# Kernel optimization log

Hardware: AMD Instinct MI355X
Metric: run time of the kernel (lower is better)

The kernel has to match this reference:

```python
import jax, jax.numpy as jnp
import numpy as np

D_K = 64
NEG = -1000000000.0

def setup_inputs() -> dict:
    key = jax.random.key(0)
    kq, kk, kv, km = jax.random.split(key, 4)
    B, H, S = 2, 16, 2048
    query = jax.random.normal(kq, (B, H, S, D_K), dtype=jnp.float32)
    k_ = jax.random.normal(kk, (B, H, S, D_K), dtype=jnp.float32)
    value = jax.random.normal(kv, (B, H, S, D_K), dtype=jnp.float32)
    mask = jax.random.randint(km, (1, 1, S, S), 0, 2, dtype=jnp.int32)
    return {"query": query, "key": k_, "value": value, "mask": mask}

def reference(query, key, value, mask):
    # scores: [B,H,S,S]
    scale = jnp.asarray(D_K ** 0.5, dtype=query.dtype)
    scores = jnp.einsum('bhqd,bhkd->bhqk', query, key) / scale
    scores = jnp.where(mask == 0, jnp.asarray(NEG, dtype=scores.dtype), scores)
    proba = jax.nn.softmax(scores, axis=-1)
    return jnp.einsum('bhqk,bhkd->bhqd', proba, value)
```

## Files before the change

kernel.cpp:

```cpp
#include <hip/hip_runtime.h>
#include <hip/hip_bf16.h>
#include <stdint.h>


#define SLEN 2048
#define DK 64
#define KVB 64
#define NTG 16
#define MFIX 13.0f
#define VPB 136
#define KIMG 9216
#define VIMG 9216
#define KOFF (512*1024)
#define VOFF (KOFF + 32*32*KIMG)
#define WSNEED ((size_t)VOFF + (size_t)32*32*VIMG)
#define TILEB (KIMG + VIMG)

typedef __attribute__((ext_vector_type(8)))  _Float16 half8;
typedef __attribute__((ext_vector_type(8)))  short    short8;
typedef __attribute__((ext_vector_type(4)))  short    s4v;
typedef __attribute__((ext_vector_type(2)))  unsigned uint2v;
typedef __attribute__((ext_vector_type(16))) float    f32x16;
typedef __attribute__((ext_vector_type(4)))  float    float4v;
typedef __attribute__((ext_vector_type(2)))  float    float2v;
typedef __attribute__((ext_vector_type(4)))  unsigned uint4v;
typedef __attribute__((ext_vector_type(4)))  int      int4v;

static __device__ __forceinline__ float fexp2(float x){
#if __has_builtin(__builtin_amdgcn_exp2f)
  return __builtin_amdgcn_exp2f(x);
#else
  float r; asm("v_exp_f32 %0, %1" : "=v"(r) : "v"(x)); return r;
#endif
}
static __device__ __forceinline__ unsigned pkh(float lo, float hi){
  return __builtin_bit_cast(unsigned, __builtin_amdgcn_cvt_pkrtz(lo, hi));
}
static __device__ __forceinline__ half8 pack8h(float4v a, float4v b, float s){
  uint4v u;
  u[0] = pkh(a[0]*s, a[1]*s);
  u[1] = pkh(a[2]*s, a[3]*s);
  u[2] = pkh(b[0]*s, b[1]*s);
  u[3] = pkh(b[2]*s, b[3]*s);
  return __builtin_bit_cast(half8, u);
}
static __device__ __forceinline__ half8 joinh(s4v a, s4v b){
  return __builtin_bit_cast(half8, __builtin_shufflevector(a, b, 0,1,2,3,4,5,6,7));
}
static __device__ __forceinline__ void gload16(const void* g, void* l){
  __builtin_amdgcn_global_load_lds(
    (const __attribute__((address_space(1))) void*)g,
    (__attribute__((address_space(3))) void*)l, 16, 0, 0);
}

__global__ __launch_bounds__(256)
void ScaledDotAttention_prep(const float* __restrict__ K, const float* __restrict__ V,
                             const int* __restrict__ mask, uint8_t* __restrict__ ws){
  __shared__ float vl[64][65];
  const int bid = blockIdx.x;
  const int i   = threadIdx.x;
  if (bid >= 1024){
    uint32_t* mtw = (uint32_t*)ws;
    int lane = i & 63;
    int wid  = i >> 6;
    int q    = (bid - 1024) * 4 + wid;
    const int* row = mask + (size_t)q * SLEN;
    #pragma unroll 4
    for (int t = 0; t < 32; ++t){
      unsigned long long b = __ballot(row[t*64 + lane] != 0);
      if (lane == 0)
        *(unsigned long long*)(mtw + (size_t)t*4096 + (size_t)q*2) = b;
    }
    return;
  }
  const int bt = bid;
  const float* Kt = K + ((size_t)(bt >> 5)*SLEN + (bt & 31)*KVB)*DK;
  const float* Vt = V + ((size_t)(bt >> 5)*SLEN + (bt & 31)*KVB)*DK;
  uint8_t* Kimg = ws + KOFF + (size_t)bt*KIMG;
  uint8_t* Vimg = ws + VOFF + (size_t)bt*VIMG;
  {
    int d8 = i & 7;
    #pragma unroll
    for (int h = 0; h < 2; ++h){
      int k = (i >> 3) + h*32;
      const float* src = Kt + k*DK + d8*8;
      float4v a = *(const float4v*)src, b = *(const float4v*)(src + 4);
      uint2v w0, w1;
      w0[0] = pkh(a[0], a[1]); w0[1] = pkh(a[2], a[3]);
      w1[0] = pkh(b[0], b[1]); w1[1] = pkh(b[2], b[3]);
      *(uint2v*)(Kimg + k*VPB + d8*16)     = w0;
      *(uint2v*)(Kimg + k*VPB + d8*16 + 8) = w1;
    }
  }
  {
    int k = i >> 2, c4 = (i & 3) * 16;
    const float* src = Vt + k*DK + c4;
    #pragma unroll
    for (int c = 0; c < 4; ++c){
      float4v x = *(const float4v*)(src + c*4);
      vl[k][c4 + c*4 + 0] = x[0]; vl[k][c4 + c*4 + 1] = x[1];
      vl[k][c4 + c*4 + 2] = x[2]; vl[k][c4 + c*4 + 3] = x[3];
    }
  }
  __syncthreads();
  {
    int d = i >> 2, k0 = (i & 3) * 16;
    #pragma unroll
    for (int c = 0; c < 4; ++c){
      uint2v w;
      w[0] = pkh(vl[k0 + c*4 + 0][d], vl[k0 + c*4 + 1][d]);
      w[1] = pkh(vl[k0 + c*4 + 2][d], vl[k0 + c*4 + 3][d]);
      *(uint2v*)(Vimg + d*VPB + k0*2 + c*8) = w;
    }
  }
}

__global__ __launch_bounds__(512, 2)
void ScaledDotAttention_attn_main(const float* __restrict__ Q,
                                  const uint8_t* __restrict__ ws,
                                  float* __restrict__ Out){
  __shared__ alignas(16) char arena[2*2*TILEB];

  const int tid  = threadIdx.x;
  const int lane = tid & 63;
  const int l31  = lane & 31;
  const int hi   = lane >> 5;
  const int wid  = __builtin_amdgcn_readfirstlane(tid >> 6);
  const int g    = wid >> 2;
  const int wq   = wid & 3;

  const int bid = blockIdx.x;
  const int xcd = bid & 7, ii = bid >> 3;
  const int bh  = xcd + 8*(ii & 3);
  const int qt  = ii >> 2;

  const float* Qb = Q + (size_t)bh*SLEN*DK;
  const int qbase = qt*128 + wq*32;
  const float C1 = 0.18033688011112042592f;

  half8 qf[4];
  {
    const float* qrow = Qb + (size_t)(qbase + l31)*DK + hi*8;
    #pragma unroll
    for (int c = 0; c < 4; ++c){
      float4v f0 = *(const float4v*)(qrow + c*16);
      float4v f1 = *(const float4v*)(qrow + c*16 + 4);
      qf[c] = pack8h(f0, f1, C1);
    }
  }

  f32x16 O0, O1;
  #pragma unroll
  for (int r = 0; r < 16; ++r){ O0[r] = 0.f; O1[r] = 0.f; }
  float lsum = 0.f;
  const float vneg = -1.0e9f;

  const uint32_t* mtw = (const uint32_t*)ws;
  auto MLOAD = [&](int it)->uint64_t{
    int kt = g*NTG + it;
    return *(const uint64_t*)(mtw + (size_t)kt*4096 + (size_t)(qbase + l31)*2);
  };

  auto STAGE = [&](int buf, int it){
    int kt = g*NTG + it;
    const uint8_t* Kg = ws + KOFF + (size_t)(bh*32 + kt)*KIMG;
    const uint8_t* Vg = ws + VOFF + (size_t)(bh*32 + kt)*VIMG;
    char* Lk = arena + g*(2*TILEB) + buf*TILEB;
    char* Lv = Lk + KIMG;
    for (int s = wq; s < 9; s += 4) gload16(Kg + s*1024 + lane*16, Lk + s*1024);
    for (int s = wq; s < 9; s += 4) gload16(Vg + s*1024 + lane*16, Lv + s*1024);
  };

  STAGE(0, 0);
  uint64_t wv = MLOAD(0);
  __syncthreads();
  int cur = 0;

  #pragma unroll 1
  for (int it = 0; it < NTG; ++it){
    if (it + 1 < NTG) STAGE(cur ^ 1, it + 1);
    uint64_t wv_next = (it + 1 < NTG) ? MLOAD(it + 1) : 0;

    const char* Klc = arena + g*(2*TILEB) + cur*TILEB;
    const char* Vtc = Klc + KIMG;

    #pragma unroll
    for (int ks = 0; ks < 2; ++ks){
      f32x16 acc;
      #pragma unroll
      for (int r = 0; r < 16; ++r) acc[r] = -MFIX;
      #pragma unroll
      for (int dc = 0; dc < 4; ++dc){
        int rowb = (ks*32 + l31)*VPB + dc*32 + hi*16;
        s4v ka = *(const s4v*)(Klc + rowb);
        s4v kb = *(const s4v*)(Klc + rowb + 8);
        acc = __builtin_amdgcn_mfma_f32_32x32x16_f16(joinh(ka, kb), qf[dc], acc, 0, 0, 0);
      }
      uint32_t w = (uint32_t)(wv >> (32*ks)) >> (4*hi);
      #pragma unroll
      for (int kc = 0; kc < 2; ++kc){
        float p[8];
        #pragma unroll
        for (int j = 0; j < 8; ++j){
          int r = kc*8 + j;
          unsigned bit = (w >> ((r & 3) + 8*(r >> 2))) & 1u;
          p[j] = fexp2(bit ? acc[r] : vneg);
        }
        lsum += ((p[0]+p[1]) + (p[2]+p[3])) + ((p[4]+p[5]) + (p[6]+p[7]));
        uint4v pw;
        pw[0] = pkh(p[0], p[1]);
        pw[1] = pkh(p[2], p[3]);
        pw[2] = pkh(p[4], p[5]);
        pw[3] = pkh(p[6], p[7]);
        half8 pf = __builtin_bit_cast(half8, pw);
        int kbyte = (ks*32 + kc*16 + 4*hi) * 2;
        #pragma unroll
        for (int hf = 0; hf < 2; ++hf){
          int d = hf*32 + l31;
          int base = d*VPB + kbyte;
          s4v a = *(const s4v*)(Vtc + base);
          s4v b = *(const s4v*)(Vtc + base + 16);
          if (hf == 0) O0 = __builtin_amdgcn_mfma_f32_32x32x16_f16(joinh(a, b), pf, O0, 0, 0, 0);
          else         O1 = __builtin_amdgcn_mfma_f32_32x32x16_f16(joinh(a, b), pf, O1, 0, 0, 0);
        }
      }
    }
    wv = wv_next;
    __syncthreads();
    cur ^= 1;
  }

  lsum = lsum + __shfl_xor(lsum, 32, 64);
  float* Mg  = (float*)arena;
  float* smL = (float*)(arena + 128*65*4);

  if (g == 1){
    float* mg = &Mg[(wq*32 + l31)*65];
    #pragma unroll
    for (int r = 0; r < 16; ++r){
      int c0 = (r & 3) + 8*(r >> 2) + 4*hi;
      mg[c0]      = O0[r];
      mg[c0 + 32] = O1[r];
    }
    if (hi == 0) smL[wq*32 + l31] = lsum;
  }
  __syncthreads();
  if (g == 0){
    float lt = lsum + smL[wq*32 + l31];
    float rinv = 1.0f / lt;
    const float* mg = &Mg[(wq*32 + l31)*65];
    float* orow = Out + ((size_t)bh*SLEN + qbase + l31)*DK;
    #pragma unroll
    for (int r = 0; r < 16; ++r){
      int c0 = (r & 3) + 8*(r >> 2) + 4*hi;
      orow[c0]      = (O0[r] + mg[c0])      * rinv;
      orow[c0 + 32] = (O1[r] + mg[c0 + 32]) * rinv;
    }
  }
}

template<bool USE_WS>
__global__ __launch_bounds__(512, 2)
void ScaledDotAttention_attn_fb(const float* __restrict__ Q, const float* __restrict__ K,
                                const float* __restrict__ V, const uint32_t* __restrict__ mtw,
                                const int* __restrict__ mask, float* __restrict__ Out)
{
  __shared__ alignas(16) unsigned short Kl[2][KVB*64];
  __shared__ alignas(16) unsigned short Vt[2][DK*(VPB/2)];
  const int tid  = threadIdx.x;
  const int lane = tid & 63;
  const int l31  = lane & 31;
  const int hi   = lane >> 5;
  const int wid  = __builtin_amdgcn_readfirstlane(tid >> 6);
  const int bid = blockIdx.x;
  const int xcd = bid & 7, ii = bid >> 3;
  const int bh  = xcd + 8*(ii & 3);
  const int qt  = ii >> 2;
  const float* Qb = Q + (size_t)bh*SLEN*DK;
  const float* Kb = K + (size_t)bh*SLEN*DK;
  const float* Vb = V + (size_t)bh*SLEN*DK;
  const int qbase = qt*256 + wid*32;
  const float C1 = 0.18033688011112042592f;
  half8 qf[4];
  {
    const float* qrow = Qb + (size_t)(qbase + l31)*DK + hi*8;
    #pragma unroll
    for (int c = 0; c < 4; ++c){
      float4v f0 = *(const float4v*)(qrow + c*16);
      float4v f1 = *(const float4v*)(qrow + c*16 + 4);
      qf[c] = pack8h(f0, f1, C1);
    }
  }
  f32x16 O0, O1;
  #pragma unroll
  for (int r = 0; r < 16; ++r){ O0[r] = 0.f; O1[r] = 0.f; }
  float lsum = 0.f;
  const float vneg = -1.0e9f;
  const int skr  = tid >> 3;
  const int sc8b = tid & 7;
  const int vd   = (tid & 31) * 2;
  const int vk   = (tid >> 5) * 4;
  float4v ka0, ka1;
  float2v vv0, vv1, vv2, vv3;
  auto LOADT = [&](int it){
    const float* kp = Kb + (size_t)it*KVB*DK + skr*DK + sc8b*8;
    ka0 = *(const float4v*)kp;  ka1 = *(const float4v*)(kp + 4);
    const float* vp = Vb + (size_t)it*KVB*DK + vk*DK + vd;
    vv0 = *(const float2v*)vp;
    vv1 = *(const float2v*)(vp + DK);
    vv2 = *(const float2v*)(vp + 2*DK);
    vv3 = *(const float2v*)(vp + 3*DK);
  };
  auto WRITE = [&](int buf){
    half8 kw = pack8h(ka0, ka1, 1.0f);
    int kaddr = (skr*128 + sc8b*16) ^ ((skr & 7) << 4);
    *(half8*)((char*)&Kl[buf][0] + kaddr) = kw;
    uint2v r0, r1;
    r0[0] = pkh(vv0[0], vv1[0]); r0[1] = pkh(vv2[0], vv3[0]);
    r1[0] = pkh(vv0[1], vv1[1]); r1[1] = pkh(vv2[1], vv3[1]);
    *(uint2v*)((char*)&Vt[buf][0] + vd*VPB + vk*2)     = r0;
    *(uint2v*)((char*)&Vt[buf][0] + (vd+1)*VPB + vk*2) = r1;
  };
  LOADT(0); WRITE(0); LOADT(1);
  __syncthreads();
  int cur = 0;
  #pragma unroll 1
  for (int it = 0; it < 32; ++it){
    if (it + 1 < 32) WRITE(cur ^ 1);
    if (it + 2 < 32) LOADT(it + 2);
    uint64_t wv = 0;
    if constexpr (USE_WS)
      wv = *(const uint64_t*)(mtw + (size_t)it*4096 + (size_t)(qbase + l31)*2);
    const unsigned short* Klc = &Kl[cur][0];
    const unsigned short* Vtc = &Vt[cur][0];
    #pragma unroll
    for (int ks = 0; ks < 2; ++ks){
      f32x16 acc;
      #pragma unroll
      for (int r = 0; r < 16; ++r) acc[r] = -MFIX;
      #pragma unroll
      for (int dc = 0; dc < 4; ++dc){
        int kaddr = ((ks*32 + l31)*128 + dc*32 + hi*16) ^ ((l31 & 7) << 4);
        half8 kf = *(const half8*)((const char*)Klc + kaddr);
        acc = __builtin_amdgcn_mfma_f32_32x32x16_f16(kf, qf[dc], acc, 0, 0, 0);
      }
      float p[16];
      if constexpr (USE_WS){
        uint32_t w = (uint32_t)(wv >> (32*ks)) >> (4*hi);
        #pragma unroll
        for (int r = 0; r < 16; ++r){
          unsigned bit = (w >> ((r & 3) + 8*(r >> 2))) & 1u;
          p[r] = fexp2(bit ? acc[r] : vneg);
        }
      } else {
        const int* mri = mask + (size_t)(qbase + l31)*SLEN + it*KVB + ks*32 + 4*hi;
        int4v g0 = *(const int4v*)(mri);
        int4v g1 = *(const int4v*)(mri + 8);
        int4v g2 = *(const int4v*)(mri + 16);
        int4v g3 = *(const int4v*)(mri + 24);
        #pragma unroll
        for (int r = 0; r < 16; ++r){
          int gi = r >> 2;
          int gv = (gi==0 ? g0[r&3] : gi==1 ? g1[r&3] : gi==2 ? g2[r&3] : g3[r&3]);
          p[r] = fexp2(gv ? acc[r] : vneg);
        }
      }
      float q0 = (p[0]+p[1]) + (p[2]+p[3]);
      float q1 = (p[4]+p[5]) + (p[6]+p[7]);
      float q2 = (p[8]+p[9]) + (p[10]+p[11]);
      float q3 = (p[12]+p[13]) + (p[14]+p[15]);
      lsum += (q0+q1) + (q2+q3);
      #pragma unroll
      for (int kc = 0; kc < 2; ++kc){
        uint4v pw;
        pw[0] = pkh(p[8*kc+0], p[8*kc+1]);
        pw[1] = pkh(p[8*kc+2], p[8*kc+3]);
        pw[2] = pkh(p[8*kc+4], p[8*kc+5]);
        pw[3] = pkh(p[8*kc+6], p[8*kc+7]);
        half8 pf = __builtin_bit_cast(half8, pw);
        int kbyte = (ks*32 + kc*16 + 4*hi) * 2;
        #pragma unroll
        for (int hf = 0; hf < 2; ++hf){
          int d = hf*32 + l31;
          int base = d*VPB + kbyte;
          s4v a = *(const s4v*)((const char*)Vtc + base);
          s4v b = *(const s4v*)((const char*)Vtc + base + 16);
          if (hf == 0) O0 = __builtin_amdgcn_mfma_f32_32x32x16_f16(joinh(a, b), pf, O0, 0, 0, 0);
          else         O1 = __builtin_amdgcn_mfma_f32_32x32x16_f16(joinh(a, b), pf, O1, 0, 0, 0);
        }
      }
    }
    __syncthreads();
    cur ^= 1;
  }
  float lt = lsum + __shfl_xor(lsum, 32, 64);
  float rinv = 1.0f / lt;
  float* orow = Out + ((size_t)bh*SLEN + qbase + l31)*DK;
  #pragma unroll
  for (int r = 0; r < 16; ++r){
    int c0 = (r & 3) + 8*(r >> 2) + 4*hi;
    orow[c0]      = O0[r] * rinv;
    orow[c0 + 32] = O1[r] * rinv;
  }
}

extern "C" void kernel_launch(void* const* d_in, const int* in_sizes, int n_in,
                              void* d_out, int out_size, void* d_ws, size_t ws_size,
                              hipStream_t stream) {
  const float* Q    = (const float*)d_in[0];
  const float* K    = (const float*)d_in[1];
  const float* V    = (const float*)d_in[2];
  const int*   mask = (const int*)d_in[3];
  float* Out = (float*)d_out;

  if (ws_size >= WSNEED) {
    uint8_t* ws = (uint8_t*)d_ws;
    ScaledDotAttention_prep<<<dim3(1536), dim3(256), 0, stream>>>(K, V, mask, ws);
    ScaledDotAttention_attn_main<<<dim3(512), dim3(512), 0, stream>>>(Q, ws, Out);
  } else if (ws_size >= (size_t)(SLEN/64) * SLEN * 2 * sizeof(uint32_t)) {
    uint32_t* mtw = (uint32_t*)d_ws;
    ScaledDotAttention_prep<<<dim3(1536), dim3(256), 0, stream>>>(K, V, mask, (uint8_t*)mtw);
    ScaledDotAttention_attn_fb<true><<<dim3(256), dim3(512), 0, stream>>>(Q, K, V, mtw, mask, Out);
  } else {
    ScaledDotAttention_attn_fb<false><<<dim3(256), dim3(512), 0, stream>>>(Q, K, V, (const uint32_t*)nullptr, mask, Out);
  }
}
```

Measured before the change: 73.57 us.

## Expand mask to fp16 bit-masks and apply via AND on packed probabilities

Adds a path, used when the workspace is large enough, that expands the int mask into per-element 16-bit all-ones/zero words. The attention kernel then exponentiates unconditionally and ANDs the packed fp16 probabilities with these words, and sums them with a dot2 instruction. This replaces the per-element bit extraction and select, and shortens the row-sum reduction. In exchange the mask becomes an 8 MB array that every head re-reads through the cache. The change also raises wave priority around the MFMA blocks with s_setprio, and restructures the PV loads to index both V halves from one base address.

```diff
diff --git a/kernel.cpp b/kernel.cpp
--- a/kernel.cpp
+++ b/kernel.cpp
@@ -11,12 +11,15 @@
 #define VPB 136
 #define KIMG 9216
 #define VIMG 9216
-#define KOFF (512*1024)
-#define VOFF (KOFF + 32*32*KIMG)
-#define WSNEED ((size_t)VOFF + (size_t)32*32*VIMG)
+#define MEXPB ((size_t)SLEN*1024*4)
+#define IMGB  ((size_t)32*32*(KIMG+VIMG))
+#define WSBIG (MEXPB + IMGB)
+#define WSMID ((size_t)512*1024 + IMGB)
+#define WSBITS ((size_t)(SLEN/64)*SLEN*2*sizeof(uint32_t))
 #define TILEB (KIMG + VIMG)
 
 typedef __attribute__((ext_vector_type(8)))  _Float16 half8;
+typedef __attribute__((ext_vector_type(2)))  _Float16 half2v;
 typedef __attribute__((ext_vector_type(8)))  short    short8;
 typedef __attribute__((ext_vector_type(4)))  short    s4v;
 typedef __attribute__((ext_vector_type(2)))  unsigned uint2v;
@@ -47,37 +50,58 @@
 static __device__ __forceinline__ half8 joinh(s4v a, s4v b){
   return __builtin_bit_cast(half8, __builtin_shufflevector(a, b, 0,1,2,3,4,5,6,7));
 }
+static __device__ __forceinline__ float dot2acc(unsigned pw, float c){
+#if __has_builtin(__builtin_amdgcn_fdot2)
+  half2v one; one[0] = (_Float16)1.0f; one[1] = (_Float16)1.0f;
+  return __builtin_amdgcn_fdot2(__builtin_bit_cast(half2v, pw), one, c, false);
+#else
+  half2v v = __builtin_bit_cast(half2v, pw);
+  return c + (float)v[0] + (float)v[1];
+#endif
+}
 static __device__ __forceinline__ void gload16(const void* g, void* l){
   __builtin_amdgcn_global_load_lds(
     (const __attribute__((address_space(1))) void*)g,
     (__attribute__((address_space(3))) void*)l, 16, 0, 0);
 }
 
+template<bool BIG>
 __global__ __launch_bounds__(256)
 void ScaledDotAttention_prep(const float* __restrict__ K, const float* __restrict__ V,
-                             const int* __restrict__ mask, uint8_t* __restrict__ ws){
+                             const int* __restrict__ mask,
+                             uint8_t* __restrict__ kimg, uint8_t* __restrict__ vimg,
+                             uint32_t* __restrict__ mw){
   __shared__ float vl[64][65];
   const int bid = blockIdx.x;
   const int i   = threadIdx.x;
   if (bid >= 1024){
-    uint32_t* mtw = (uint32_t*)ws;
     int lane = i & 63;
-    int wid  = i >> 6;
-    int q    = (bid - 1024) * 4 + wid;
+    int wd   = i >> 6;
+    int q    = (bid - 1024) * 4 + wd;
     const int* row = mask + (size_t)q * SLEN;
-    #pragma unroll 4
-    for (int t = 0; t < 32; ++t){
-      unsigned long long b = __ballot(row[t*64 + lane] != 0);
-      if (lane == 0)
-        *(unsigned long long*)(mtw + (size_t)t*4096 + (size_t)q*2) = b;
+    if constexpr (BIG){
+      uint32_t* out = mw + (size_t)q*1024 + lane*16;
+      const int* src = row + lane*32;
+      #pragma unroll
+      for (int t = 0; t < 16; ++t){
+        int i0 = src[2*t], i1 = src[2*t + 1];
+        out[t] = (i0 ? 0xFFFFu : 0u) | (i1 ? 0xFFFF0000u : 0u);
+      }
+    } else {
+      #pragma unroll 4
+      for (int t = 0; t < 32; ++t){
+        unsigned long long b = __ballot(row[t*64 + lane] != 0);
+        if (lane == 0)
+          *(unsigned long long*)(mw + (size_t)t*4096 + (size_t)q*2) = b;
+      }
     }
     return;
   }
   const int bt = bid;
   const float* Kt = K + ((size_t)(bt >> 5)*SLEN + (bt & 31)*KVB)*DK;
   const float* Vt = V + ((size_t)(bt >> 5)*SLEN + (bt & 31)*KVB)*DK;
-  uint8_t* Kimg = ws + KOFF + (size_t)bt*KIMG;
-  uint8_t* Vimg = ws + VOFF + (size_t)bt*VIMG;
+  uint8_t* Kimg = kimg + (size_t)bt*KIMG;
+  uint8_t* Vimg = vimg + (size_t)bt*VIMG;
   {
     int d8 = i & 7;
     #pragma unroll
@@ -115,9 +139,12 @@
   }
 }
 
+template<bool BIG>
 __global__ __launch_bounds__(512, 2)
 void ScaledDotAttention_attn_main(const float* __restrict__ Q,
-                                  const uint8_t* __restrict__ ws,
+                                  const uint8_t* __restrict__ kimg,
+                                  const uint8_t* __restrict__ vimg,
+                                  const uint32_t* __restrict__ mptr,
                                   float* __restrict__ Out){
   __shared__ alignas(16) char arena[2*2*TILEB];
 
@@ -155,16 +182,16 @@
   float lsum = 0.f;
   const float vneg = -1.0e9f;
 
-  const uint32_t* mtw = (const uint32_t*)ws;
+  const uint32_t* mrow = BIG ? (mptr + (size_t)(qbase + l31)*1024) : nullptr;
   auto MLOAD = [&](int it)->uint64_t{
     int kt = g*NTG + it;
-    return *(const uint64_t*)(mtw + (size_t)kt*4096 + (size_t)(qbase + l31)*2);
+    return *(const uint64_t*)(mptr + (size_t)kt*4096 + (size_t)(qbase + l31)*2);
   };
 
   auto STAGE = [&](int buf, int it){
     int kt = g*NTG + it;
-    const uint8_t* Kg = ws + KOFF + (size_t)(bh*32 + kt)*KIMG;
-    const uint8_t* Vg = ws + VOFF + (size_t)(bh*32 + kt)*VIMG;
+    const uint8_t* Kg = kimg + (size_t)(bh*32 + kt)*KIMG;
+    const uint8_t* Vg = vimg + (size_t)(bh*32 + kt)*VIMG;
     char* Lk = arena + g*(2*TILEB) + buf*TILEB;
     char* Lv = Lk + KIMG;
     for (int s = wq; s < 9; s += 4) gload16(Kg + s*1024 + lane*16, Lk + s*1024);
@@ -172,23 +199,25 @@
   };
 
   STAGE(0, 0);
-  uint64_t wv = MLOAD(0);
+  uint64_t wv = BIG ? 0 : MLOAD(0);
   __syncthreads();
   int cur = 0;
 
   #pragma unroll 1
   for (int it = 0; it < NTG; ++it){
     if (it + 1 < NTG) STAGE(cur ^ 1, it + 1);
-    uint64_t wv_next = (it + 1 < NTG) ? MLOAD(it + 1) : 0;
+    uint64_t wv_next = (!BIG && it + 1 < NTG) ? MLOAD(it + 1) : 0;
 
     const char* Klc = arena + g*(2*TILEB) + cur*TILEB;
     const char* Vtc = Klc + KIMG;
+    const uint32_t* mit = BIG ? (mrow + (g*NTG + it)*32) : nullptr;
 
     #pragma unroll
     for (int ks = 0; ks < 2; ++ks){
       f32x16 acc;
       #pragma unroll
       for (int r = 0; r < 16; ++r) acc[r] = -MFIX;
+      __builtin_amdgcn_s_setprio(1);
       #pragma unroll
       for (int dc = 0; dc < 4; ++dc){
         int rowb = (ks*32 + l31)*VPB + dc*32 + hi*16;
@@ -196,36 +225,58 @@
         s4v kb = *(const s4v*)(Klc + rowb + 8);
         acc = __builtin_amdgcn_mfma_f32_32x32x16_f16(joinh(ka, kb), qf[dc], acc, 0, 0, 0);
       }
-      uint32_t w = (uint32_t)(wv >> (32*ks)) >> (4*hi);
+      __builtin_amdgcn_s_setprio(0);
+
+      uint32_t w = 0;
+      if constexpr (!BIG) w = (uint32_t)(wv >> (32*ks)) >> (4*hi);
+
       #pragma unroll
       for (int kc = 0; kc < 2; ++kc){
-        float p[8];
-        #pragma unroll
-        for (int j = 0; j < 8; ++j){
-          int r = kc*8 + j;
-          unsigned bit = (w >> ((r & 3) + 8*(r >> 2))) & 1u;
-          p[j] = fexp2(bit ? acc[r] : vneg);
+        uint4v pw;
+        if constexpr (BIG){
+          float p[8];
+          #pragma unroll
+          for (int j = 0; j < 8; ++j) p[j] = fexp2(acc[kc*8 + j]);
+          pw[0] = pkh(p[0], p[1]);
+          pw[1] = pkh(p[2], p[3]);
+          pw[2] = pkh(p[4], p[5]);
+          pw[3] = pkh(p[6], p[7]);
+          uint2v ma = *(const uint2v*)(mit + ks*16 + kc*8 + 2*hi);
+          uint2v mb = *(const uint2v*)(mit + ks*16 + kc*8 + 2*hi + 4);
+          pw[0] &= ma[0]; pw[1] &= ma[1];
+          pw[2] &= mb[0]; pw[3] &= mb[1];
+          lsum = dot2acc(pw[0], lsum);
+          lsum = dot2acc(pw[1], lsum);
+          lsum = dot2acc(pw[2], lsum);
+          lsum = dot2acc(pw[3], lsum);
+        } else {
+          float p[8];
+          #pragma unroll
+          for (int j = 0; j < 8; ++j){
+            int r = kc*8 + j;
+            unsigned bit = (w >> ((r & 3) + 8*(r >> 2))) & 1u;
+            p[j] = fexp2(bit ? acc[r] : vneg);
+          }
+          lsum += ((p[0]+p[1]) + (p[2]+p[3])) + ((p[4]+p[5]) + (p[6]+p[7]));
+          pw[0] = pkh(p[0], p[1]);
+          pw[1] = pkh(p[2], p[3]);
+          pw[2] = pkh(p[4], p[5]);
+          pw[3] = pkh(p[6], p[7]);
         }
-        lsum += ((p[0]+p[1]) + (p[2]+p[3])) + ((p[4]+p[5]) + (p[6]+p[7]));
-        uint4v pw;
-        pw[0] = pkh(p[0], p[1]);
-        pw[1] = pkh(p[2], p[3]);
-        pw[2] = pkh(p[4], p[5]);
-        pw[3] = pkh(p[6], p[7]);
         half8 pf = __builtin_bit_cast(half8, pw);
         int kbyte = (ks*32 + kc*16 + 4*hi) * 2;
-        #pragma unroll
-        for (int hf = 0; hf < 2; ++hf){
-          int d = hf*32 + l31;
-          int base = d*VPB + kbyte;
-          s4v a = *(const s4v*)(Vtc + base);
-          s4v b = *(const s4v*)(Vtc + base + 16);
-          if (hf == 0) O0 = __builtin_amdgcn_mfma_f32_32x32x16_f16(joinh(a, b), pf, O0, 0, 0, 0);
-          else         O1 = __builtin_amdgcn_mfma_f32_32x32x16_f16(joinh(a, b), pf, O1, 0, 0, 0);
-        }
-      }
-    }
-    wv = wv_next;
+        int d0 = l31*VPB + kbyte;
+        s4v a0 = *(const s4v*)(Vtc + d0);
+        s4v b0 = *(const s4v*)(Vtc + d0 + 16);
+        s4v a1 = *(const s4v*)(Vtc + d0 + 32*VPB);
+        s4v b1 = *(const s4v*)(Vtc + d0 + 32*VPB + 16);
+        __builtin_amdgcn_s_setprio(1);
+        O0 = __builtin_amdgcn_mfma_f32_32x32x16_f16(joinh(a0, b0), pf, O0, 0, 0, 0);
+        O1 = __builtin_amdgcn_mfma_f32_32x32x16_f16(joinh(a1, b1), pf, O1, 0, 0, 0);
+        __builtin_amdgcn_s_setprio(0);
+      }
+    }
+    if constexpr (!BIG) wv = wv_next;
     __syncthreads();
     cur ^= 1;
   }
@@ -412,16 +463,30 @@
   const float* V    = (const float*)d_in[2];
   const int*   mask = (const int*)d_in[3];
   float* Out = (float*)d_out;
-
-  if (ws_size >= WSNEED) {
-    uint8_t* ws = (uint8_t*)d_ws;
-    ScaledDotAttention_prep<<<dim3(1536), dim3(256), 0, stream>>>(K, V, mask, ws);
-    ScaledDotAttention_attn_main<<<dim3(512), dim3(512), 0, stream>>>(Q, ws, Out);
-  } else if (ws_size >= (size_t)(SLEN/64) * SLEN * 2 * sizeof(uint32_t)) {
+  uint8_t* ws = (uint8_t*)d_ws;
+
+  if (ws_size >= WSBIG) {
+    uint8_t* kimg = ws + MEXPB;
+    uint8_t* vimg = kimg + (size_t)32*32*KIMG;
+    ScaledDotAttention_prep<true><<<dim3(1536), dim3(256), 0, stream>>>(
+        K, V, mask, kimg, vimg, (uint32_t*)ws);
+    ScaledDotAttention_attn_main<true><<<dim3(512), dim3(512), 0, stream>>>(
+        Q, kimg, vimg, (const uint32_t*)ws, Out);
+  } else if (ws_size >= WSMID) {
+    uint8_t* kimg = ws + 512*1024;
+    uint8_t* vimg = kimg + (size_t)32*32*KIMG;
+    ScaledDotAttention_prep<false><<<dim3(1536), dim3(256), 0, stream>>>(
+        K, V, mask, kimg, vimg, (uint32_t*)ws);
+    ScaledDotAttention_attn_main<false><<<dim3(512), dim3(512), 0, stream>>>(
+        Q, kimg, vimg, (const uint32_t*)ws, Out);
+  } else if (ws_size >= WSBITS) {
     uint32_t* mtw = (uint32_t*)d_ws;
-    ScaledDotAttention_prep<<<dim3(1536), dim3(256), 0, stream>>>(K, V, mask, (uint8_t*)mtw);
-    ScaledDotAttention_attn_fb<true><<<dim3(256), dim3(512), 0, stream>>>(Q, K, V, mtw, mask, Out);
+    ScaledDotAttention_prep<false><<<dim3(512), dim3(256), 0, stream>>>(
+        K, V, mask, nullptr, nullptr, mtw);
+    ScaledDotAttention_attn_fb<true><<<dim3(256), dim3(512), 0, stream>>>(
+        Q, K, V, mtw, mask, Out);
   } else {
-    ScaledDotAttention_attn_fb<false><<<dim3(256), dim3(512), 0, stream>>>(Q, K, V, (const uint32_t*)nullptr, mask, Out);
-  }
-}
+    ScaledDotAttention_attn_fb<false><<<dim3(256), dim3(512), 0, stream>>>(
+        Q, K, V, (const uint32_t*)nullptr, mask, Out);
+  }
+}
```

After: 94.49 us. 28.4% more time.
